# Kernel optimization log

Measured on AMD Instinct MI355X. Metric: run time of the kernel, lower is better.

## Reference

```python
import jax, jax.numpy as jnp
import numpy as np

BUCKETS = 32
DIM = 1024
HEADS = 16
TEMP = 0.75
SINK_ITERS = 7
LOG_EPS = 1e-6
GUMBEL_EPS = 1e-4


def _sinkhorn(r, n_iters):
    # iterative row/col log-normalization, then exp (matches torch loop)
    for _ in range(n_iters):
        r = r - jax.scipy.special.logsumexp(r, axis=2, keepdims=True)
        r = r - jax.scipy.special.logsumexp(r, axis=1, keepdims=True)
    return jnp.exp(r)


def setup_inputs() -> dict:
    key = jax.random.key(0)
    kq, kk, kv, kw, kg = jax.random.split(key, 5)
    B, H, T, DH = 4, 16, 4096, 64
    q = jax.random.normal(kq, (B, H, T, DH), jnp.float32)
    k = jax.random.normal(kk, (B, H, T, DH), jnp.float32)
    v = jax.random.normal(kv, (B, H, T, DH), jnp.float32)
    sort_w = jax.random.normal(kw, (1, H, DH, BUCKETS), jnp.float32)
    u = jax.random.uniform(kg, (B * H, BUCKETS, BUCKETS), jnp.float32, 0.0, 1.0)
    gumbel_noise = -jnp.log(-jnp.log(u + GUMBEL_EPS) + GUMBEL_EPS)
    return {"q": q, "k": k, "v": v, "sort_w": sort_w, "gumbel_noise": gumbel_noise}


def reference(q, k, v, sort_w, gumbel_noise):
    b, h, t, dh = q.shape
    bh = b * h
    bsz = t // BUCKETS  # tokens per bucket
    # bucket: (bh, buckets, bsz, dh)
    qb = q.reshape(bh, BUCKETS, bsz, dh)
    kb = k.reshape(bh, BUCKETS, bsz, dh)
    vb = v.reshape(bh, BUCKETS, bsz, dh)
    # bucket summaries for routing
    b_k_r = kb.sum(axis=2)  # (bh, buckets, dh)
    e_w = jnp.broadcast_to(sort_w, (b, h, dh, BUCKETS)).reshape(bh, dh, BUCKETS)
    R = jnp.log(jax.nn.relu(jnp.einsum('bud,bdv->buv', b_k_r, e_w)) + LOG_EPS)
    R = (R + gumbel_noise) / TEMP
    R = _sinkhorn(R, SINK_ITERS)  # soft permutation matrix (bh, buckets, buckets)
    R = jnp.tril(R, -1)  # causal: only attend to strictly earlier buckets
    # soft-permute key/value buckets
    k_re = jnp.einsum('buv,bvtd->butd', R, kb)
    v_re = jnp.einsum('buv,bvtd->butd', R, vb)
    bk = jnp.concatenate([k_re, kb], axis=2)  # (bh, buckets, 2*bsz, dh)
    bv = jnp.concatenate([v_re, vb], axis=2)
    dots = jnp.einsum('buie,buje->buij', qb, bk) * (DIM ** -0.5)
    attn = jax.nn.softmax(dots, axis=-1)
    out = jnp.einsum('buij,buje->buie', attn, bv)  # (bh, buckets, bsz, dh)
    return out.reshape(b, h, t, dh)
```

## Files before the change

### kernel.cpp

```cpp
#include <hip/hip_runtime.h>
#include <hip/hip_bf16.h>

#define BUCKETS 32
#define BSZ 128
#define DH 64
#define TEMPINV 1.3333333333333333f
#define SINK_ITERS 7
#define LOG_EPS 1e-6f
#define SCALE 0.03125f

typedef short bf16x8 __attribute__((ext_vector_type(8)));
typedef float f32x4 __attribute__((ext_vector_type(4)));

__device__ __forceinline__ void bf8_to_f32(const uint4 x, float* f) {
    f[0] = __uint_as_float(x.x << 16);
    f[1] = __uint_as_float(x.x & 0xffff0000u);
    f[2] = __uint_as_float(x.y << 16);
    f[3] = __uint_as_float(x.y & 0xffff0000u);
    f[4] = __uint_as_float(x.z << 16);
    f[5] = __uint_as_float(x.z & 0xffff0000u);
    f[6] = __uint_as_float(x.w << 16);
    f[7] = __uint_as_float(x.w & 0xffff0000u);
}

__device__ __forceinline__ unsigned f2bf(float f) {
    unsigned x = __float_as_uint(f);
    return (x + 0x7fffu + ((x >> 16) & 1u)) >> 16;
}

__device__ __forceinline__ uint4 packbf8(const float* f) {
    uint4 r;
    r.x = f2bf(f[0]) | (f2bf(f[1]) << 16);
    r.y = f2bf(f[2]) | (f2bf(f[3]) << 16);
    r.z = f2bf(f[4]) | (f2bf(f[5]) << 16);
    r.w = f2bf(f[6]) | (f2bf(f[7]) << 16);
    return r;
}

__device__ __forceinline__ void load_lds16(const uint4* g, uint4* l) {
    __builtin_amdgcn_global_load_lds(
        (const __attribute__((address_space(1))) unsigned int*)g,
        (__attribute__((address_space(3))) unsigned int*)l, 16, 0, 0);
}

__global__ __launch_bounds__(256) void bksum_kernel(
    const float* __restrict__ kptr, float* __restrict__ bkr)
{
    const int t = blockIdx.x;
    const int tid = threadIdx.x;
    __shared__ float4 part[16][17];
    const float4* k4 = (const float4*)kptr + (size_t)t * 2048;
    const int c4 = tid & 15, rg = tid >> 4;
    float4 s; s.x = 0.f; s.y = 0.f; s.z = 0.f; s.w = 0.f;
    for (int r = rg; r < 128; r += 16) {
        float4 a = k4[r * 16 + c4];
        s.x += a.x; s.y += a.y; s.z += a.z; s.w += a.w;
    }
    part[rg][c4] = s;
    __syncthreads();
    if (tid < 16) {
        float4 acc = part[0][tid];
        for (int g = 1; g < 16; ++g) {
            float4 p = part[g][tid];
            acc.x += p.x; acc.y += p.y; acc.z += p.z; acc.w += p.w;
        }
        ((float4*)bkr)[t * 16 + tid] = acc;
    }
}

__global__ __launch_bounds__(256) void sinkhorn_kernel(
    const float* __restrict__ bkrp,
    const float* __restrict__ swptr,
    const float* __restrict__ gptr,
    float* __restrict__ Rout)
{
    const int b = blockIdx.x;
    const int h = b & 15;
    const int tid = threadIdx.x;

    __shared__ float bk[BUCKETS][DH];
    __shared__ float sw[DH][BUCKETS];
    __shared__ float R[BUCKETS][BUCKETS + 1];

    for (int o = tid; o < DH * BUCKETS; o += 256)
        sw[o >> 5][o & 31] = swptr[h * DH * BUCKETS + o];
    for (int o = tid; o < BUCKETS * DH; o += 256)
        bk[o >> 6][o & 63] = bkrp[b * 2048 + o];
    __syncthreads();

    for (int o = tid; o < BUCKETS * BUCKETS; o += 256) {
        const int uu = o >> 5, vv = o & 31;
        float dot = 0.f;
        for (int d = 0; d < DH; ++d) dot = fmaf(bk[uu][d], sw[d][vv], dot);
        const float g = gptr[b * 1024 + o];
        R[uu][vv] = (logf(fmaxf(dot, 0.f) + LOG_EPS) + g) * TEMPINV;
    }
    __syncthreads();

    for (int it = 0; it < SINK_ITERS; ++it) {
        if (tid < BUCKETS) {
            float m = -1e30f;
            for (int j = 0; j < BUCKETS; ++j) m = fmaxf(m, R[tid][j]);
            float s = 0.f;
            for (int j = 0; j < BUCKETS; ++j) s += expf(R[tid][j] - m);
            const float lse = m + logf(s);
            for (int j = 0; j < BUCKETS; ++j) R[tid][j] -= lse;
        }
        __syncthreads();
        if (tid < BUCKETS) {
            float m = -1e30f;
            for (int j = 0; j < BUCKETS; ++j) m = fmaxf(m, R[j][tid]);
            float s = 0.f;
            for (int j = 0; j < BUCKETS; ++j) s += expf(R[j][tid] - m);
            const float lse = m + logf(s);
            for (int j = 0; j < BUCKETS; ++j) R[j][tid] -= lse;
        }
        __syncthreads();
    }

    for (int o = tid; o < BUCKETS * BUCKETS; o += 256) {
        const int uu = o >> 5, vv = o & 31;
        Rout[b * 1024 + o] = (vv < uu) ? expf(R[uu][vv]) : 0.f;
    }
}

__global__ __launch_bounds__(256) void reshuffle2_kernel(
    const float* __restrict__ kptr,
    const float* __restrict__ vptr,
    const float* __restrict__ Rmat,
    uint4* __restrict__ kimg,
    uint4* __restrict__ vimg)
{
    const int j0 = blockIdx.x;
    const int b  = blockIdx.y;
    const int tid = threadIdx.x;
    const int u = tid >> 3, c8 = tid & 7;

    __shared__ float ls[32][8][64];
    __shared__ float lr[32][33];

    for (int o = tid; o < 1024; o += 256)
        lr[o >> 5][o & 31] = Rmat[b * 1024 + o];

    float4* ls4 = (float4*)ls;

    {
        const float4* kb4 = (const float4*)kptr + (size_t)b * 65536 + j0 * 128;
        for (int it = 0; it < 16; ++it) {
            const int idx = it * 256 + tid;
            const int v = idx >> 7, i = idx & 127;
            ls4[v * 128 + i] = kb4[v * 2048 + i];
        }
    }
    __syncthreads();
    {
        float ka[8][8];
        #pragma unroll
        for (int r = 0; r < 8; ++r)
            #pragma unroll
            for (int t = 0; t < 8; ++t) ka[r][t] = 0.f;
        for (int vv = 0; vv < u; ++vv) {
            const float rw = lr[u][vv];
            #pragma unroll
            for (int r = 0; r < 8; ++r)
                #pragma unroll
                for (int t = 0; t < 8; ++t)
                    ka[r][t] = fmaf(rw, ls[vv][r][c8 * 8 + t], ka[r][t]);
        }
        uint4* kdst = kimg + ((size_t)b * 32 + u) * 2048;
        #pragma unroll
        for (int r = 0; r < 8; ++r) {
            kdst[(j0 * 8 + r) * 8 + (c8 ^ r)] = packbf8(ka[r]);
            float o8[8];
            #pragma unroll
            for (int t = 0; t < 8; ++t) o8[t] = ls[u][r][c8 * 8 + t];
            kdst[(128 + j0 * 8 + r) * 8 + (c8 ^ r)] = packbf8(o8);
        }
    }
    __syncthreads();

    {
        const float4* vb4 = (const float4*)vptr + (size_t)b * 65536 + j0 * 128;
        for (int it = 0; it < 16; ++it) {
            const int idx = it * 256 + tid;
            const int v = idx >> 7, i = idx & 127;
            ls4[v * 128 + i] = vb4[v * 2048 + i];
        }
    }
    __syncthreads();
    {
        float va[8][8];
        #pragma unroll
        for (int r = 0; r < 8; ++r)
            #pragma unroll
            for (int t = 0; t < 8; ++t) va[r][t] = 0.f;
        for (int vv = 0; vv < u; ++vv) {
            const float rw = lr[u][vv];
            #pragma unroll
            for (int r = 0; r < 8; ++r)
                #pragma unroll
                for (int t = 0; t < 8; ++t)
                    va[r][t] = fmaf(rw, ls[vv][r][c8 * 8 + t], va[r][t]);
        }
        uint4* vdst = vimg + ((size_t)b * 32 + u) * 2048;
        #pragma unroll
        for (int t = 0; t < 8; ++t) {
            const int blk = c8 * 8 + (t ^ c8);
            uint4 wre;
            wre.x = f2bf(va[0][t]) | (f2bf(va[1][t]) << 16);
            wre.y = f2bf(va[2][t]) | (f2bf(va[3][t]) << 16);
            wre.z = f2bf(va[4][t]) | (f2bf(va[5][t]) << 16);
            wre.w = f2bf(va[6][t]) | (f2bf(va[7][t]) << 16);
            vdst[j0 * 64 + blk] = wre;
            uint4 wor;
            wor.x = f2bf(ls[u][0][c8 * 8 + t]) | (f2bf(ls[u][1][c8 * 8 + t]) << 16);
            wor.y = f2bf(ls[u][2][c8 * 8 + t]) | (f2bf(ls[u][3][c8 * 8 + t]) << 16);
            wor.z = f2bf(ls[u][4][c8 * 8 + t]) | (f2bf(ls[u][5][c8 * 8 + t]) << 16);
            wor.w = f2bf(ls[u][6][c8 * 8 + t]) | (f2bf(ls[u][7][c8 * 8 + t]) << 16);
            vdst[(16 + j0) * 64 + blk] = wor;
        }
    }
}

__global__ __launch_bounds__(128) void attn_fallback(
    const float* __restrict__ qptr,
    const float* __restrict__ kptr,
    const float* __restrict__ vptr,
    const float* __restrict__ Rmat,
    float4* __restrict__ optr)
{
    const int u = blockIdx.x;
    const int b = blockIdx.y;
    const int tid = threadIdx.x;

    __shared__ uint4 sbk[2048];
    __shared__ uint4 sbv[2048];

    const float4* k4 = (const float4*)kptr + (size_t)b * 65536;
    const float4* v4 = (const float4*)vptr + (size_t)b * 65536;
    const float4* q4 = (const float4*)qptr + (size_t)b * 65536;

    const float* Rrow = Rmat + (b * BUCKETS + u) * BUCKETS;
    for (int o = tid; o < 1024; o += 128) {
        float ka[8] = {0.f,0.f,0.f,0.f,0.f,0.f,0.f,0.f};
        float va[8] = {0.f,0.f,0.f,0.f,0.f,0.f,0.f,0.f};
        for (int vv = 0; vv < u; ++vv) {
            const float r = Rrow[vv];
            float4 a = k4[vv * 2048 + 2 * o], c = k4[vv * 2048 + 2 * o + 1];
            ka[0] = fmaf(r, a.x, ka[0]); ka[1] = fmaf(r, a.y, ka[1]);
            ka[2] = fmaf(r, a.z, ka[2]); ka[3] = fmaf(r, a.w, ka[3]);
            ka[4] = fmaf(r, c.x, ka[4]); ka[5] = fmaf(r, c.y, ka[5]);
            ka[6] = fmaf(r, c.z, ka[6]); ka[7] = fmaf(r, c.w, ka[7]);
            float4 av = v4[vv * 2048 + 2 * o], cv = v4[vv * 2048 + 2 * o + 1];
            va[0] = fmaf(r, av.x, va[0]); va[1] = fmaf(r, av.y, va[1]);
            va[2] = fmaf(r, av.z, va[2]); va[3] = fmaf(r, av.w, va[3]);
            va[4] = fmaf(r, cv.x, va[4]); va[5] = fmaf(r, cv.y, va[5]);
            va[6] = fmaf(r, cv.z, va[6]); va[7] = fmaf(r, cv.w, va[7]);
        }
        sbk[o] = packbf8(ka);
        sbv[o] = packbf8(va);
        float4 a = k4[u * 2048 + 2 * o], c = k4[u * 2048 + 2 * o + 1];
        float f[8] = {a.x,a.y,a.z,a.w,c.x,c.y,c.z,c.w};
        sbk[1024 + o] = packbf8(f);
        float4 av = v4[u * 2048 + 2 * o], cv = v4[u * 2048 + 2 * o + 1];
        float g[8] = {av.x,av.y,av.z,av.w,cv.x,cv.y,cv.z,cv.w};
        sbv[1024 + o] = packbf8(g);
    }
    __syncthreads();

    const int i = tid;
    float qr[64];
    const float4* qrow = q4 + (u * 128 + i) * 16;
    for (int d4 = 0; d4 < 16; ++d4) {
        float4 t = qrow[d4];
        qr[d4 * 4 + 0] = t.x; qr[d4 * 4 + 1] = t.y;
        qr[d4 * 4 + 2] = t.z; qr[d4 * 4 + 3] = t.w;
    }

    float acc[64];
    for (int d = 0; d < 64; ++d) acc[d] = 0.f;
    float l = 0.f;

    for (int j = 0; j < 256; ++j) {
        float s = 0.f;
        for (int d8 = 0; d8 < 8; ++d8) {
            float f[8];
            bf8_to_f32(sbk[j * 8 + d8], f);
            for (int t = 0; t < 8; ++t) s = fmaf(qr[d8 * 8 + t], f[t], s);
        }
        const float p = __expf(s * SCALE);
        l += p;
        for (int d8 = 0; d8 < 8; ++d8) {
            float f[8];
            bf8_to_f32(sbv[j * 8 + d8], f);
            for (int t = 0; t < 8; ++t)
                acc[d8 * 8 + t] = fmaf(p, f[t], acc[d8 * 8 + t]);
        }
    }

    const float inv = 1.f / l;
    float4* orow = optr + (size_t)b * 65536 + (u * 128 + i) * 16;
    for (int d4 = 0; d4 < 16; ++d4) {
        float4 t;
        t.x = acc[d4 * 4 + 0] * inv;
        t.y = acc[d4 * 4 + 1] * inv;
        t.z = acc[d4 * 4 + 2] * inv;
        t.w = acc[d4 * 4 + 3] * inv;
        orow[d4] = t;
    }
}

__global__ __launch_bounds__(256) void attn_mfma2(
    const float* __restrict__ qptr,
    const uint4* __restrict__ kimg,
    const uint4* __restrict__ vimg,
    float* __restrict__ optr)
{
    const int u = blockIdx.x;
    const int b = blockIdx.y;
    const int tid = threadIdx.x;
    const int lane = tid & 63;
    const int w = tid >> 6;
    const int lg = lane >> 4;
    const int lr = lane & 15;

    __shared__ uint4 sK[2048];
    __shared__ uint4 sV[2048];
    __shared__ uint4 sP[1024];

    const size_t tile = (size_t)b * 32 + u;
    const uint4* gk = kimg + tile * 2048;
    const uint4* gv = vimg + tile * 2048;

    #pragma unroll
    for (int it = 0; it < 8; ++it)
        load_lds16(gk + it * 256 + tid, &sK[it * 256 + (w << 6)]);
    #pragma unroll
    for (int it = 0; it < 8; ++it)
        load_lds16(gv + it * 256 + tid, &sV[it * 256 + (w << 6)]);

    const float* qbase = qptr + (size_t)b * 262144 + (size_t)u * 8192;
    bf16x8 qf[2][2];
    #pragma unroll
    for (int mt = 0; mt < 2; ++mt)
        #pragma unroll
        for (int c = 0; c < 2; ++c) {
            const int row = w * 32 + mt * 16 + lr;
            const float4* qr = (const float4*)(qbase + row * 64 + (c * 4 + lg) * 8);
            float4 a = qr[0], cc = qr[1];
            float f[8] = {a.x * SCALE, a.y * SCALE, a.z * SCALE, a.w * SCALE,
                          cc.x * SCALE, cc.y * SCALE, cc.z * SCALE, cc.w * SCALE};
            uint4 tq = packbf8(f);
            qf[mt][c] = *(bf16x8*)&tq;
        }
    __syncthreads();

    uint4* sPw = sP + w * 256;
    unsigned short* sPh = (unsigned short*)sPw;

    f32x4 acc[2][4];
    float lsum[2][4];
    #pragma unroll
    for (int mt = 0; mt < 2; ++mt) {
        #pragma unroll
        for (int nt = 0; nt < 4; ++nt) {
            acc[mt][nt][0] = 0.f; acc[mt][nt][1] = 0.f;
            acc[mt][nt][2] = 0.f; acc[mt][nt][3] = 0.f;
        }
        #pragma unroll
        for (int r = 0; r < 4; ++r) lsum[mt][r] = 0.f;
    }

    for (int kb = 0; kb < 4; ++kb) {
        bf16x8 kf[4][2];
        #pragma unroll
        for (int nt = 0; nt < 4; ++nt)
            #pragma unroll
            for (int c = 0; c < 2; ++c) {
                const int j = kb * 64 + nt * 16 + lr;
                const int dcu = c * 4 + lg;
                uint4 t = sK[j * 8 + (dcu ^ (j & 7))];
                kf[nt][c] = *(bf16x8*)&t;
            }
        f32x4 s[2][4];
        #pragma unroll
        for (int mt = 0; mt < 2; ++mt)
            #pragma unroll
            for (int nt = 0; nt < 4; ++nt) {
                s[mt][nt][0] = 0.f; s[mt][nt][1] = 0.f;
                s[mt][nt][2] = 0.f; s[mt][nt][3] = 0.f;
            }
        __builtin_amdgcn_s_setprio(1);
        #pragma unroll
        for (int c = 0; c < 2; ++c)
            #pragma unroll
            for (int mt = 0; mt < 2; ++mt)
                #pragma unroll
                for (int nt = 0; nt < 4; ++nt)
                    s[mt][nt] = __builtin_amdgcn_mfma_f32_16x16x32_bf16(
                        qf[mt][c], kf[nt][c], s[mt][nt], 0, 0, 0);
        __builtin_amdgcn_s_setprio(0);

        #pragma unroll
        for (int mt = 0; mt < 2; ++mt)
            #pragma unroll
            for (int nt = 0; nt < 4; ++nt)
                #pragma unroll
                for (int r = 0; r < 4; ++r) {
                    const float p = __expf(s[mt][nt][r]);
                    lsum[mt][r] += p;
                    const int row = mt * 16 + lg * 4 + r;
                    const int col = nt * 16 + lr;
                    sPh[row * 64 + (((col >> 3) ^ (row & 7)) << 3) + (col & 7)] =
                        (unsigned short)f2bf(p);
                }
        asm volatile("s_waitcnt lgkmcnt(0)" ::: "memory");
        __builtin_amdgcn_sched_barrier(0);

        bf16x8 pf[2][2];
        #pragma unroll
        for (int mt = 0; mt < 2; ++mt)
            #pragma unroll
            for (int c = 0; c < 2; ++c) {
                const int row = mt * 16 + lr;
                const int dcu = c * 4 + lg;
                uint4 t = sPw[row * 8 + (dcu ^ (row & 7))];
                pf[mt][c] = *(bf16x8*)&t;
            }
        bf16x8 vf[4][2];
        #pragma unroll
        for (int nt = 0; nt < 4; ++nt)
            #pragma unroll
            for (int c = 0; c < 2; ++c) {
                const int p = kb * 8 + c * 4 + lg;
                const int d = nt * 16 + lr;
                const int blk = (d >> 3) * 8 + ((d & 7) ^ ((d >> 3) & 7));
                uint4 t = sV[p * 64 + blk];
                vf[nt][c] = *(bf16x8*)&t;
            }
        __builtin_amdgcn_s_setprio(1);
        #pragma unroll
        for (int c = 0; c < 2; ++c)
            #pragma unroll
            for (int mt = 0; mt < 2; ++mt)
                #pragma unroll
                for (int nt = 0; nt < 4; ++nt)
                    acc[mt][nt] = __builtin_amdgcn_mfma_f32_16x16x32_bf16(
                        pf[mt][c], vf[nt][c], acc[mt][nt], 0, 0, 0);
        __builtin_amdgcn_s_setprio(0);
    }

    #pragma unroll
    for (int mt = 0; mt < 2; ++mt)
        #pragma unroll
        for (int r = 0; r < 4; ++r) {
            float sum = lsum[mt][r];
            sum += __shfl_xor(sum, 1);
            sum += __shfl_xor(sum, 2);
            sum += __shfl_xor(sum, 4);
            sum += __shfl_xor(sum, 8);
            const float inv = 1.f / sum;
            const int row = mt * 16 + lg * 4 + r;
            float* orow = optr + (size_t)b * 262144 +
                          (size_t)(u * 128 + w * 32 + row) * 64;
            #pragma unroll
            for (int nt = 0; nt < 4; ++nt)
                orow[nt * 16 + lr] = acc[mt][nt][r] * inv;
        }
}

extern "C" void kernel_launch(void* const* d_in, const int* in_sizes, int n_in,
                              void* d_out, int out_size, void* d_ws, size_t ws_size,
                              hipStream_t stream) {
    const float* q  = (const float*)d_in[0];
    const float* k  = (const float*)d_in[1];
    const float* v  = (const float*)d_in[2];
    const float* sw = (const float*)d_in[3];
    const float* g  = (const float*)d_in[4];

    float* R    = (float*)d_ws;
    float* bkr  = (float*)((char*)d_ws + 262144);
    uint4* kimg = (uint4*)((char*)d_ws + 1048576);
    uint4* vimg = (uint4*)((char*)d_ws + 1048576 + 67108864);
    const bool big_ws = (ws_size >= (size_t)1048576 + 2u * 67108864u);

    bksum_kernel<<<dim3(2048), dim3(256), 0, stream>>>(k, bkr);
    sinkhorn_kernel<<<dim3(64), dim3(256), 0, stream>>>(bkr, sw, g, R);
    if (big_ws) {
        reshuffle2_kernel<<<dim3(16, 64), dim3(256), 0, stream>>>(k, v, R, kimg, vimg);
        attn_mfma2<<<dim3(32, 64), dim3(256), 0, stream>>>(q, kimg, vimg, (float*)d_out);
    } else {
        attn_fallback<<<dim3(32, 64), dim3(128), 0, stream>>>(q, k, v, R, (float4*)d_out);
    }
}
```

Before: 328.8 us.

## Parallelize sinkhorn, balance reshuffle work, stage V via LDS, double-buffer attention K/V

Sinkhorn row/column normalization now uses all 256 threads with 8-lane shuffle reductions instead of 32 serial threads. The reshuffle kernel interleaves buckets across waves so the triangular causal work is spread evenly, and stages the V image in shared memory for coalesced global stores. The attention kernel loads Q early and double-buffers K/V tiles per key block, overlapping loads with MFMA compute through explicit vmcnt waits and barriers. The cost is extra barriers, smaller LDS buffers and more hand-tuned synchronization that could be fragile.

```diff
diff --git a/kernel.cpp b/kernel.cpp
--- a/kernel.cpp
+++ b/kernel.cpp
@@ -97,25 +97,36 @@
     }
     __syncthreads();
 
+    const int rr = tid >> 3, sub = tid & 7;
     for (int it = 0; it < SINK_ITERS; ++it) {
-        if (tid < BUCKETS) {
-            float m = -1e30f;
-            for (int j = 0; j < BUCKETS; ++j) m = fmaxf(m, R[tid][j]);
-            float s = 0.f;
-            for (int j = 0; j < BUCKETS; ++j) s += expf(R[tid][j] - m);
+        {
+            float vals[4];
+            float m = -1e30f, s = 0.f;
+            #pragma unroll
+            for (int q = 0; q < 4; ++q) { vals[q] = R[rr][sub * 4 + q]; m = fmaxf(m, vals[q]); }
+            m = fmaxf(m, __shfl_xor(m, 1)); m = fmaxf(m, __shfl_xor(m, 2)); m = fmaxf(m, __shfl_xor(m, 4));
+            #pragma unroll
+            for (int q = 0; q < 4; ++q) s += expf(vals[q] - m);
+            s += __shfl_xor(s, 1); s += __shfl_xor(s, 2); s += __shfl_xor(s, 4);
             const float lse = m + logf(s);
-            for (int j = 0; j < BUCKETS; ++j) R[tid][j] -= lse;
-        }
-        __syncthreads();
-        if (tid < BUCKETS) {
-            float m = -1e30f;
-            for (int j = 0; j < BUCKETS; ++j) m = fmaxf(m, R[j][tid]);
-            float s = 0.f;
-            for (int j = 0; j < BUCKETS; ++j) s += expf(R[j][tid] - m);
+            #pragma unroll
+            for (int q = 0; q < 4; ++q) R[rr][sub * 4 + q] = vals[q] - lse;
+            __syncthreads();
+        }
+        {
+            float vals[4];
+            float m = -1e30f, s = 0.f;
+            #pragma unroll
+            for (int q = 0; q < 4; ++q) { vals[q] = R[sub * 4 + q][rr]; m = fmaxf(m, vals[q]); }
+            m = fmaxf(m, __shfl_xor(m, 1)); m = fmaxf(m, __shfl_xor(m, 2)); m = fmaxf(m, __shfl_xor(m, 4));
+            #pragma unroll
+            for (int q = 0; q < 4; ++q) s += expf(vals[q] - m);
+            s += __shfl_xor(s, 1); s += __shfl_xor(s, 2); s += __shfl_xor(s, 4);
             const float lse = m + logf(s);
-            for (int j = 0; j < BUCKETS; ++j) R[j][tid] -= lse;
-        }
-        __syncthreads();
+            #pragma unroll
+            for (int q = 0; q < 4; ++q) R[sub * 4 + q][rr] = vals[q] - lse;
+            __syncthreads();
+        }
     }
 
     for (int o = tid; o < BUCKETS * BUCKETS; o += 256) {
@@ -124,7 +135,7 @@
     }
 }
 
-__global__ __launch_bounds__(256) void reshuffle2_kernel(
+__global__ __launch_bounds__(256) void reshuffle4_kernel(
     const float* __restrict__ kptr,
     const float* __restrict__ vptr,
     const float* __restrict__ Rmat,
@@ -134,7 +145,8 @@
     const int j0 = blockIdx.x;
     const int b  = blockIdx.y;
     const int tid = threadIdx.x;
-    const int u = tid >> 3, c8 = tid & 7;
+    const int w = tid >> 6, g = (tid >> 3) & 7, c8 = tid & 7;
+    const int u = g * 4 + w;
 
     __shared__ float ls[32][8][64];
     __shared__ float lr[32][33];
@@ -160,12 +172,12 @@
             #pragma unroll
             for (int t = 0; t < 8; ++t) ka[r][t] = 0.f;
         for (int vv = 0; vv < u; ++vv) {
-            const float rw = lr[u][vv];
+            const float rwt = lr[u][vv];
             #pragma unroll
             for (int r = 0; r < 8; ++r)
                 #pragma unroll
                 for (int t = 0; t < 8; ++t)
-                    ka[r][t] = fmaf(rw, ls[vv][r][c8 * 8 + t], ka[r][t]);
+                    ka[r][t] = fmaf(rwt, ls[vv][r][c8 * 8 + t], ka[r][t]);
         }
         uint4* kdst = kimg + ((size_t)b * 32 + u) * 2048;
         #pragma unroll
@@ -189,20 +201,30 @@
     }
     __syncthreads();
     {
+        uint4 wor[8];
+        #pragma unroll
+        for (int t = 0; t < 8; ++t) {
+            wor[t].x = f2bf(ls[u][0][c8 * 8 + t]) | (f2bf(ls[u][1][c8 * 8 + t]) << 16);
+            wor[t].y = f2bf(ls[u][2][c8 * 8 + t]) | (f2bf(ls[u][3][c8 * 8 + t]) << 16);
+            wor[t].z = f2bf(ls[u][4][c8 * 8 + t]) | (f2bf(ls[u][5][c8 * 8 + t]) << 16);
+            wor[t].w = f2bf(ls[u][6][c8 * 8 + t]) | (f2bf(ls[u][7][c8 * 8 + t]) << 16);
+        }
         float va[8][8];
         #pragma unroll
         for (int r = 0; r < 8; ++r)
             #pragma unroll
             for (int t = 0; t < 8; ++t) va[r][t] = 0.f;
         for (int vv = 0; vv < u; ++vv) {
-            const float rw = lr[u][vv];
+            const float rwt = lr[u][vv];
             #pragma unroll
             for (int r = 0; r < 8; ++r)
                 #pragma unroll
                 for (int t = 0; t < 8; ++t)
-                    va[r][t] = fmaf(rw, ls[vv][r][c8 * 8 + t], va[r][t]);
-        }
-        uint4* vdst = vimg + ((size_t)b * 32 + u) * 2048;
+                    va[r][t] = fmaf(rwt, ls[vv][r][c8 * 8 + t], va[r][t]);
+        }
+        __syncthreads();
+
+        uint4* img = (uint4*)ls;
         #pragma unroll
         for (int t = 0; t < 8; ++t) {
             const int blk = c8 * 8 + (t ^ c8);
@@ -211,13 +233,16 @@
             wre.y = f2bf(va[2][t]) | (f2bf(va[3][t]) << 16);
             wre.z = f2bf(va[4][t]) | (f2bf(va[5][t]) << 16);
             wre.w = f2bf(va[6][t]) | (f2bf(va[7][t]) << 16);
-            vdst[j0 * 64 + blk] = wre;
-            uint4 wor;
-            wor.x = f2bf(ls[u][0][c8 * 8 + t]) | (f2bf(ls[u][1][c8 * 8 + t]) << 16);
-            wor.y = f2bf(ls[u][2][c8 * 8 + t]) | (f2bf(ls[u][3][c8 * 8 + t]) << 16);
-            wor.z = f2bf(ls[u][4][c8 * 8 + t]) | (f2bf(ls[u][5][c8 * 8 + t]) << 16);
-            wor.w = f2bf(ls[u][6][c8 * 8 + t]) | (f2bf(ls[u][7][c8 * 8 + t]) << 16);
-            vdst[(16 + j0) * 64 + blk] = wor;
+            img[u * 64 + blk] = wre;
+            img[2048 + u * 64 + blk] = wor[t];
+        }
+        __syncthreads();
+
+        for (int o = tid; o < 2048; o += 256) {
+            const int uu = o >> 6, blk = o & 63;
+            const size_t tb = ((size_t)b * 32 + uu) * 2048;
+            vimg[tb + j0 * 64 + blk] = img[o];
+            vimg[tb + (16 + j0) * 64 + blk] = img[2048 + o];
         }
     }
 }
@@ -263,8 +288,8 @@
         float f[8] = {a.x,a.y,a.z,a.w,c.x,c.y,c.z,c.w};
         sbk[1024 + o] = packbf8(f);
         float4 av = v4[u * 2048 + 2 * o], cv = v4[u * 2048 + 2 * o + 1];
-        float g[8] = {av.x,av.y,av.z,av.w,cv.x,cv.y,cv.z,cv.w};
-        sbv[1024 + o] = packbf8(g);
+        float gg[8] = {av.x,av.y,av.z,av.w,cv.x,cv.y,cv.z,cv.w};
+        sbv[1024 + o] = packbf8(gg);
     }
     __syncthreads();
 
@@ -310,7 +335,7 @@
     }
 }
 
-__global__ __launch_bounds__(256) void attn_mfma2(
+__global__ __launch_bounds__(256) void attn_mfma3(
     const float* __restrict__ qptr,
     const uint4* __restrict__ kimg,
     const uint4* __restrict__ vimg,
@@ -324,36 +349,47 @@
     const int lg = lane >> 4;
     const int lr = lane & 15;
 
-    __shared__ uint4 sK[2048];
-    __shared__ uint4 sV[2048];
+    __shared__ uint4 sK[2][512];
+    __shared__ uint4 sV[2][512];
     __shared__ uint4 sP[1024];
 
     const size_t tile = (size_t)b * 32 + u;
     const uint4* gk = kimg + tile * 2048;
     const uint4* gv = vimg + tile * 2048;
 
+    const float* qbase = qptr + (size_t)b * 262144 + (size_t)u * 8192;
+    float4 qa[2][2], qc[2][2];
     #pragma unroll
-    for (int it = 0; it < 8; ++it)
-        load_lds16(gk + it * 256 + tid, &sK[it * 256 + (w << 6)]);
-    #pragma unroll
-    for (int it = 0; it < 8; ++it)
-        load_lds16(gv + it * 256 + tid, &sV[it * 256 + (w << 6)]);
-
-    const float* qbase = qptr + (size_t)b * 262144 + (size_t)u * 8192;
+    for (int mt = 0; mt < 2; ++mt)
+        #pragma unroll
+        for (int c = 0; c < 2; ++c) {
+            const int row = w * 32 + mt * 16 + lr;
+            const float4* qr = (const float4*)(qbase + row * 64 + (c * 4 + lg) * 8);
+            qa[mt][c] = qr[0];
+            qc[mt][c] = qr[1];
+        }
+
+#define STAGE_KB(kbi, bufi) do { \
+        load_lds16(gk + (kbi) * 512 +   0 + tid, &sK[bufi][  0 + (w << 6)]); \
+        load_lds16(gk + (kbi) * 512 + 256 + tid, &sK[bufi][256 + (w << 6)]); \
+        load_lds16(gv + (kbi) * 512 +   0 + tid, &sV[bufi][  0 + (w << 6)]); \
+        load_lds16(gv + (kbi) * 512 + 256 + tid, &sV[bufi][256 + (w << 6)]); \
+    } while (0)
+    STAGE_KB(0, 0);
+    STAGE_KB(1, 1);
+
     bf16x8 qf[2][2];
     #pragma unroll
     for (int mt = 0; mt < 2; ++mt)
         #pragma unroll
         for (int c = 0; c < 2; ++c) {
-            const int row = w * 32 + mt * 16 + lr;
-            const float4* qr = (const float4*)(qbase + row * 64 + (c * 4 + lg) * 8);
-            float4 a = qr[0], cc = qr[1];
-            float f[8] = {a.x * SCALE, a.y * SCALE, a.z * SCALE, a.w * SCALE,
-                          cc.x * SCALE, cc.y * SCALE, cc.z * SCALE, cc.w * SCALE};
+            float f[8] = {qa[mt][c].x * SCALE, qa[mt][c].y * SCALE,
+                          qa[mt][c].z * SCALE, qa[mt][c].w * SCALE,
+                          qc[mt][c].x * SCALE, qc[mt][c].y * SCALE,
+                          qc[mt][c].z * SCALE, qc[mt][c].w * SCALE};
             uint4 tq = packbf8(f);
             qf[mt][c] = *(bf16x8*)&tq;
         }
-    __syncthreads();
 
     uint4* sPw = sP + w * 256;
     unsigned short* sPh = (unsigned short*)sPw;
@@ -371,15 +407,24 @@
         for (int r = 0; r < 4; ++r) lsum[mt][r] = 0.f;
     }
 
+    #pragma unroll
     for (int kb = 0; kb < 4; ++kb) {
+        const uint4* bK = sK[kb & 1];
+        const uint4* bV = sV[kb & 1];
+
+        if (kb < 3) asm volatile("s_waitcnt vmcnt(4)" ::: "memory");
+        else        asm volatile("s_waitcnt vmcnt(0)" ::: "memory");
+        __builtin_amdgcn_s_barrier();
+        __builtin_amdgcn_sched_barrier(0);
+
         bf16x8 kf[4][2];
         #pragma unroll
         for (int nt = 0; nt < 4; ++nt)
             #pragma unroll
             for (int c = 0; c < 2; ++c) {
-                const int j = kb * 64 + nt * 16 + lr;
+                const int jj = nt * 16 + lr;
                 const int dcu = c * 4 + lg;
-                uint4 t = sK[j * 8 + (dcu ^ (j & 7))];
+                uint4 t = bK[jj * 8 + (dcu ^ (jj & 7))];
                 kf[nt][c] = *(bf16x8*)&t;
             }
         f32x4 s[2][4];
@@ -432,10 +477,10 @@
         for (int nt = 0; nt < 4; ++nt)
             #pragma unroll
             for (int c = 0; c < 2; ++c) {
-                const int p = kb * 8 + c * 4 + lg;
+                const int pp = c * 4 + lg;
                 const int d = nt * 16 + lr;
                 const int blk = (d >> 3) * 8 + ((d & 7) ^ ((d >> 3) & 7));
-                uint4 t = sV[p * 64 + blk];
+                uint4 t = bV[pp * 64 + blk];
                 vf[nt][c] = *(bf16x8*)&t;
             }
         __builtin_amdgcn_s_setprio(1);
@@ -448,7 +493,13 @@
                     acc[mt][nt] = __builtin_amdgcn_mfma_f32_16x16x32_bf16(
                         pf[mt][c], vf[nt][c], acc[mt][nt], 0, 0, 0);
         __builtin_amdgcn_s_setprio(0);
-    }
+
+        __builtin_amdgcn_sched_barrier(0);
+        __builtin_amdgcn_s_barrier();
+        __builtin_amdgcn_sched_barrier(0);
+        if (kb < 2) STAGE_KB(kb + 2, kb & 1);
+    }
+#undef STAGE_KB
 
     #pragma unroll
     for (int mt = 0; mt < 2; ++mt)
@@ -487,8 +538,8 @@
     bksum_kernel<<<dim3(2048), dim3(256), 0, stream>>>(k, bkr);
     sinkhorn_kernel<<<dim3(64), dim3(256), 0, stream>>>(bkr, sw, g, R);
     if (big_ws) {
-        reshuffle2_kernel<<<dim3(16, 64), dim3(256), 0, stream>>>(k, v, R, kimg, vimg);
-        attn_mfma2<<<dim3(32, 64), dim3(256), 0, stream>>>(q, kimg, vimg, (float*)d_out);
+        reshuffle4_kernel<<<dim3(16, 64), dim3(256), 0, stream>>>(k, v, R, kimg, vimg);
+        attn_mfma3<<<dim3(32, 64), dim3(256), 0, stream>>>(q, kimg, vimg, (float*)d_out);
     } else {
         attn_fallback<<<dim3(32, 64), dim3(128), 0, stream>>>(q, k, v, R, (float4*)d_out);
     }
```

After: 344.2 us. +4.7%, slower.
